# Optimization experiments

Measured on AMD Instinct MI355X. Metric: run time of the kernel, lower is better.

The kernel has to match this reference:

```python
import jax, jax.numpy as jnp
import numpy as np

B, N, D, H = 4, 2048, 256, 4
DH = D // H          # 64
SCALE = DH ** (-0.5)
LN_EPS = 1e-5


def setup_inputs() -> dict:
    key = jax.random.key(0)
    ks = jax.random.split(key, 16)
    g = lambda k, shape, fan_in: jax.random.normal(k, shape, jnp.float32) / np.sqrt(fan_in)
    # Weights stored as [in, out] (pre-transposed vs torch Linear)
    return {
        "x0": jax.random.normal(ks[0], (B, N, D), jnp.float32),
        "x1": jax.random.normal(ks[1], (B, N, D), jnp.float32),
        "Wqk": g(ks[2], (D, D), D), "bqk": jnp.zeros((D,), jnp.float32),
        "Wv": g(ks[3], (D, D), D), "bv": jnp.zeros((D,), jnp.float32),
        "Wout": g(ks[4], (D, D), D), "bout": jnp.zeros((D,), jnp.float32),
        "Wf1": g(ks[5], (2 * D, 2 * D), 2 * D), "bf1": jnp.zeros((2 * D,), jnp.float32),
        "ln_g": jnp.ones((2 * D,), jnp.float32), "ln_b": jnp.zeros((2 * D,), jnp.float32),
        "Wf2": g(ks[6], (2 * D, D), 2 * D), "bf2": jnp.zeros((D,), jnp.float32),
    }


def _split_heads(t):
    # [B,N,D] -> [B,H,N,DH]
    b, n, _ = t.shape
    return t.reshape(b, n, H, DH).transpose(0, 2, 1, 3)


def _merge_heads(t):
    # [B,H,N,DH] -> [B,N,D]
    b, h, n, dh = t.shape
    return t.transpose(0, 2, 1, 3).reshape(b, n, h * dh)


def _layernorm(x, g, b):
    mu = jnp.mean(x, axis=-1, keepdims=True)
    var = jnp.mean(jnp.square(x - mu), axis=-1, keepdims=True)
    return (x - mu) * jax.lax.rsqrt(var + LN_EPS) * g + b


def reference(x0, x1, Wqk, bqk, Wv, bv, Wout, bout, Wf1, bf1, ln_g, ln_b, Wf2, bf2):
    qk0 = _split_heads(x0 @ Wqk + bqk)   # [B,H,N,DH]
    qk1 = _split_heads(x1 @ Wqk + bqk)
    v0 = _split_heads(x0 @ Wv + bv)
    v1 = _split_heads(x1 @ Wv + bv)

    ss = SCALE ** 0.5
    sim = jnp.einsum('bhid,bhjd->bhij', qk0 * ss, qk1 * ss)  # shared score matrix
    attn01 = jax.nn.softmax(sim, axis=-1)   # normalize over j
    attn10 = jax.nn.softmax(sim, axis=-2)   # normalize over i (== softmax(sim^T) transposed)
    m0 = jnp.einsum('bhij,bhjd->bhid', attn01, v1)
    m1 = jnp.einsum('bhji,bhjd->bhid', attn10, v0)

    m0 = _merge_heads(m0) @ Wout + bout   # [B,N,D]
    m1 = _merge_heads(m1) @ Wout + bout

    def ffn(x):
        h = x @ Wf1 + bf1                 # [B,N,2D]
        h = jax.nn.gelu(_layernorm(h, ln_g, ln_b), approximate=False)
        return h @ Wf2 + bf2              # [B,N,D]

    y0 = x0 + ffn(jnp.concatenate([x0, m0], axis=-1))
    y1 = x1 + ffn(jnp.concatenate([x1, m1], axis=-1))
    return (y0, y1)
```

## Files before the change

kernel.cpp:

```cpp
#include <hip/hip_runtime.h>
#include <hip/hip_bf16.h>
#include <math.h>

typedef __bf16 bf16;
typedef __attribute__((ext_vector_type(8))) __bf16 bf16x8;
typedef __attribute__((ext_vector_type(4))) __bf16 bf16x4;
typedef __attribute__((ext_vector_type(2))) __bf16 bf16x2;
typedef __attribute__((ext_vector_type(4))) float f32x4;
typedef __attribute__((ext_vector_type(16))) float f32x16;
typedef __attribute__((ext_vector_type(4))) unsigned u32x4;

#define MFMA(a,b,c)   __builtin_amdgcn_mfma_f32_16x16x32_bf16(a,b,c,0,0,0)
#define MFMA32(a,b,c) __builtin_amdgcn_mfma_f32_32x32x16_bf16(a,b,c,0,0,0)

static constexpr int Bb = 4, Nn = 2048, Hh = 4;
static constexpr float SS2 = 0.4246609001440095f;

__device__ __forceinline__ void lds16(const bf16* src, bf16* dst) {
  __builtin_amdgcn_global_load_lds(
      (const __attribute__((address_space(1))) void*)src,
      (__attribute__((address_space(3))) void*)dst, 16, 0, 0);
}

__device__ __forceinline__ f32x16 zero16() {
  f32x16 t;
#pragma unroll
  for (int i = 0; i < 16; ++i) t[i] = 0.f;
  return t;
}

__global__ __launch_bounds__(256) void prep_k(
    const float* Wqk, const float* Wv, const float* Wout, const float* bout,
    const float* Wf1, const float* Wf2, const float* x0, const float* x1,
    bf16* wqkv_t, bf16* wout_b, bf16* wfold_t, bf16* wf1b_t, bf16* wf2_t,
    bf16* xb0, bf16* xb1) {
  int id = blockIdx.x * 256 + threadIdx.x;
  if (id < 65536) { int k = id >> 8, n = id & 255; wqkv_t[n*256 + k] = (bf16)Wqk[id]; return; }
  id -= 65536;
  if (id < 65536) { int k = id >> 8, n = id & 255; wqkv_t[(256 + n)*256 + k] = (bf16)Wv[id]; return; }
  id -= 65536;
  if (id < 98304) {
    if (id < 65536) { wout_b[id] = (bf16)Wout[id]; }
    else { int id3 = id - 65536; int r = id3 >> 8, k = id3 & 255;
           wout_b[(256 + r)*256 + k] = (r == 0) ? (bf16)bout[k] : (bf16)0.f; }
    return; }
  id -= 98304;
  if (id < 131072) { int o = id & 511, k = id >> 9; wfold_t[o*512 + k] = (bf16)Wf1[k*512 + o]; return; }
  id -= 131072;
  if (id < 131072) { int o = id & 511, k = id >> 9; wf1b_t[o*256 + k] = (bf16)Wf1[(256 + k)*512 + o]; return; }
  id -= 131072;
  if (id < 131072) { int k = id >> 8, n = id & 255; wf2_t[n*512 + k] = (bf16)Wf2[id]; return; }
  id -= 131072;
  if (id < 1048576) {
    const float* xs = (id < 524288) ? x0 : x1;
    bf16* xd = (id < 524288) ? xb0 : xb1;
    int j = (id < 524288) ? id : id - 524288;
    f32x4 v = *reinterpret_cast<const f32x4*>(&xs[(size_t)j * 4]);
    bf16x4 o; o[0] = (bf16)v[0]; o[1] = (bf16)v[1]; o[2] = (bf16)v[2]; o[3] = (bf16)v[3];
    *reinterpret_cast<bf16x4*>(&xd[(size_t)j * 4]) = o;
  }
}

template<int MODE, int BN, int MINW, int REMAP>
__global__ __launch_bounds__(256, MINW) void gemm_k(
    const bf16* Aa0, const bf16* Aa1, const bf16* Ac0, const bf16* Ac1,
    const bf16* Wt, const float* bias,
    bf16* ob0, bf16* ob1, float* of0, float* of1,
    const float* res0, const float* res1) {
  constexpr int KD  = (MODE == 3 || MODE == 4) ? 512 : 256;
  constexpr int LDA = (MODE == 4) ? 512 : 256;
  constexpr int NKC = KD / 64;
  constexpr int NF  = BN / 32;

  int bx = blockIdx.x, by = blockIdx.y, bz = blockIdx.z;
  if constexpr (REMAP) {
    int id = blockIdx.x + 64 * (blockIdx.y + 4 * blockIdx.z);
    bx = ((id & 7) << 3) + ((id >> 3) & 7);
    by = (id >> 6) & 3;
    bz = id >> 8;
  }

  const bf16* Aa = bz ? Aa1 : Aa0;
  const bf16* Ac = bz ? Ac1 : Ac0;
  bf16*  ob = bz ? ob1 : ob0;
  float* of = bz ? of1 : of0;
  const float* res = bz ? res1 : res0;

  const int tid = threadIdx.x;
  const int lane = tid & 63;
  const int w = tid >> 6;
  const int wr = w >> 1, wc = w & 1;
  const int m0r = bx * 128;
  const int n0 = by * BN;
  const int r15 = lane & 15, g = lane >> 4, rb = r15 & 7;
  const int l3 = lane >> 3, l7 = lane & 7;
  const int swzc = (l7 ^ l3) * 8;

  __shared__ bf16 At[2][8192];
  __shared__ bf16 Bt[2][BN * 64];

  const bf16* aA = Aa + (size_t)(m0r + w*32 + l3) * LDA + swzc;
  const bf16* aC = (MODE == 3) ? (Ac + (size_t)(m0r + w*32 + l3) * 256 + swzc) : nullptr;
  const bf16* bB = Wt + (size_t)(n0 + w*(BN/4) + l3) * KD + swzc;
  const int adst = (w*32) * 64;
  const int bdst = (w*(BN/4)) * 64;

  auto stage = [&](int buf, int kc) {
    const bf16* ab; int kcol;
    if constexpr (MODE == 3) {
      if (kc < 4) { ab = aA; kcol = kc * 64; } else { ab = aC; kcol = (kc - 4) * 64; }
    } else { ab = aA; kcol = kc * 64; }
#pragma unroll
    for (int i = 0; i < 4; i++)
      lds16(ab + kcol + (size_t)i * 8 * LDA, &At[buf][adst + i*512]);
#pragma unroll
    for (int i = 0; i < NF; i++)
      lds16(bB + kc*64 + (size_t)i * 8 * KD, &Bt[buf][bdst + i*512]);
  };

  f32x4 acc[4][NF];
#pragma unroll
  for (int i = 0; i < 4; i++)
#pragma unroll
    for (int j = 0; j < NF; j++) acc[i][j] = f32x4{0.f, 0.f, 0.f, 0.f};

  const int rx0 = ((0*4 + g) ^ rb) << 4;
  const int rx1 = ((1*4 + g) ^ rb) << 4;

  auto compute = [&](int cur) {
    const char* Ap = (const char*)&At[cur][0];
    const char* Bp = (const char*)&Bt[cur][0];
    __builtin_amdgcn_s_setprio(1);
#pragma unroll
    for (int ks = 0; ks < 2; ++ks) {
      const int rx = ks ? rx1 : rx0;
      bf16x8 af[4], bfr[NF];
#pragma unroll
      for (int mf = 0; mf < 4; ++mf)
        af[mf] = *reinterpret_cast<const bf16x8*>(Ap + (wr*64 + mf*16 + r15) * 128 + rx);
#pragma unroll
      for (int nf = 0; nf < NF; ++nf)
        bfr[nf] = *reinterpret_cast<const bf16x8*>(Bp + (wc*(BN/2) + nf*16 + r15) * 128 + rx);
#pragma unroll
      for (int mf = 0; mf < 4; ++mf)
#pragma unroll
        for (int nf = 0; nf < NF; ++nf)
          acc[mf][nf] = MFMA(af[mf], bfr[nf], acc[mf][nf]);
    }
    __builtin_amdgcn_s_setprio(0);
  };

  stage(0, 0);
  int cur = 0;
  for (int kc = 0; kc < NKC - 1; ++kc) {
    stage(cur ^ 1, kc + 1);
    if constexpr (NF == 4) asm volatile("s_waitcnt vmcnt(8)" ::: "memory");
    else                   asm volatile("s_waitcnt vmcnt(6)" ::: "memory");
    __builtin_amdgcn_sched_barrier(0);
    __builtin_amdgcn_s_barrier();
    __builtin_amdgcn_sched_barrier(0);
    compute(cur);
    asm volatile("s_waitcnt lgkmcnt(0)" ::: "memory");
    __builtin_amdgcn_sched_barrier(0);
    __builtin_amdgcn_s_barrier();
    __builtin_amdgcn_sched_barrier(0);
    cur ^= 1;
  }
  asm volatile("s_waitcnt vmcnt(0)" ::: "memory");
  __builtin_amdgcn_sched_barrier(0);
  __builtin_amdgcn_s_barrier();
  __builtin_amdgcn_sched_barrier(0);
  compute(cur);

#pragma unroll
  for (int mf = 0; mf < 4; ++mf)
#pragma unroll
    for (int nf = 0; nf < NF; ++nf) {
      f32x4 c = acc[mf][nf];
      int cg = n0 + wc*(BN/2) + nf*16 + r15;
#pragma unroll
      for (int r = 0; r < 4; ++r) {
        int rg = m0r + wr*64 + mf*16 + g*4 + r;
        if constexpr (MODE == 5) {
          int b = rg >> 11, n = rg & 2047;
          if (cg < 256) {
            float val = (c[r] + bias[cg]) * SS2;
            int h = cg >> 6, dh = cg & 63;
            ob[(((size_t)(b*Hh + h)) * Nn + n) * 64 + dh] = (bf16)val;
          } else {
            int c2 = cg - 256;
            float val = c[r] + res[c2];
            int h = c2 >> 6, dh = c2 & 63;
            ((bf16*)of)[(((size_t)(b*Hh + h)) * 64 + dh) * Nn + n] = (bf16)val;
          }
        } else if constexpr (MODE == 6) {
          if (rg < 256) ob[(size_t)cg * 512 + 256 + rg] = (bf16)c[r];
          else if (rg == 256) of[cg] = c[r] + bias[cg];
        } else if constexpr (MODE == 3) {
          ob[(size_t)rg * 512 + cg] = (bf16)(c[r] + bias[cg]);
        } else {
          of[(size_t)rg * 256 + cg] = c[r] + bias[cg] + (float)Ac[(size_t)rg * 256 + cg];
        }
      }
    }
}

__global__ __launch_bounds__(512, 4) void attn_k(
    const bf16* qks0, const bf16* qks1, const bf16* vT0, const bf16* vT1,
    bf16* m0o, bf16* m1o) {
  const int B = blockIdx.x + 16 * (blockIdx.y + 16 * blockIdx.z);
  const int xcd = B & 7, kk = B >> 3;
  const int group = 4 * xcd + (kk >> 4);
  const int it = kk & 15;
  const int bh = group & 15, dir = group >> 4;

  const bf16* Q  = (dir ? qks1 : qks0) + (size_t)bh * (Nn * 64);
  const bf16* Kp = (dir ? qks0 : qks1) + (size_t)bh * (Nn * 64);
  const bf16* Vp = (dir ? vT0  : vT1 ) + (size_t)bh * (64 * Nn);
  bf16* out = dir ? m1o : m0o;
  const int b = bh >> 2, h = bh & 3;

  const int tid = threadIdx.x, lane = tid & 63, w = tid >> 6;
  const int ig = w >> 1, hj = w & 1;
  const int l31 = lane & 31, hi = lane >> 5, xr = l31 & 7;
  const int iw = it * 128 + ig * 32;

  __shared__ char smem[65536];
  bf16* KV = (bf16*)smem;
  const int kbase = hj * 8192;
  const int vbase = 16384 + hj * 8192;

  bf16x8 qf[4];
#pragma unroll
  for (int kt = 0; kt < 4; ++kt)
    qf[kt] = *reinterpret_cast<const bf16x8*>(
        &Q[(size_t)(iw + l31) * 64 + kt*16 + hi*8]);

  bf16x8 ones;
#pragma unroll
  for (int i = 0; i < 8; ++i) ones[i] = (bf16)1.0f;

  f32x16 acc[2]; acc[0] = zero16(); acc[1] = zero16();
  f32x16 rsacc = zero16();

  const int l3 = lane >> 3, l7 = lane & 7;
  const int swz = ((l7 ^ l3) * 8);
  const bf16* ks0 = Kp + (size_t)(ig*16 +     l3) * 64 + swz;
  const bf16* ks1 = Kp + (size_t)(ig*16 + 8 + l3) * 64 + swz;
  const bf16* vs0 = Vp + (size_t)(ig*16 +     l3) * 2048 + swz;
  const bf16* vs1 = Vp + (size_t)(ig*16 + 8 + l3) * 2048 + swz;
  const int kd0 = (ig*16    ) * 64;
  const int kd1 = (ig*16 + 8) * 64;

  auto stage = [&](int buf, int j0) {
    lds16(ks0 + (size_t)j0 * 64, KV + kbase + buf*4096 + kd0);
    lds16(ks1 + (size_t)j0 * 64, KV + kbase + buf*4096 + kd1);
    lds16(vs0 + j0,              KV + vbase + buf*4096 + kd0);
    lds16(vs1 + j0,              KV + vbase + buf*4096 + kd1);
  };

  int kby[2][4], vby[2][4];
#pragma unroll
  for (int jm = 0; jm < 2; ++jm)
#pragma unroll
    for (int kt = 0; kt < 4; ++kt)
      kby[jm][kt] = (jm*32 + l31) * 128 + (((2*kt + hi) ^ xr) << 4);
#pragma unroll
  for (int nt = 0; nt < 2; ++nt)
#pragma unroll
    for (int gg = 0; gg < 4; ++gg)
      vby[nt][gg] = (nt*32 + l31) * 128 + (((2*gg + hi) ^ xr) << 4);

  auto compute_tile = [&](int cur) {
    const char* Kb = (const char*)(KV + kbase + cur*4096);
    const char* Vb = (const char*)(KV + vbase + cur*4096);
    f32x16 st[2];
    __builtin_amdgcn_s_setprio(1);
#pragma unroll
    for (int jm = 0; jm < 2; ++jm) {
      f32x16 t = zero16();
#pragma unroll
      for (int kt = 0; kt < 4; ++kt) {
        bf16x8 kf = *reinterpret_cast<const bf16x8*>(Kb + kby[jm][kt]);
        t = MFMA32(kf, qf[kt], t);
      }
      st[jm] = t;
    }
    __builtin_amdgcn_s_setprio(0);
    bf16x8 pa[4];
#pragma unroll
    for (int jm = 0; jm < 2; ++jm) {
      unsigned dw[8];
#pragma unroll
      for (int s = 0; s < 8; ++s) {
        float e0 = __builtin_amdgcn_exp2f(st[jm][2*s]);
        float e1 = __builtin_amdgcn_exp2f(st[jm][2*s + 1]);
        asm("v_cvt_pk_bf16_f32 %0, %1, %2" : "=v"(dw[s]) : "v"(e0), "v"(e1));
      }
#pragma unroll
      for (int kt2 = 0; kt2 < 2; ++kt2) {
        unsigned a0 = dw[4*kt2 + 0], b0 = dw[4*kt2 + 2];
        unsigned a1 = dw[4*kt2 + 1], b1 = dw[4*kt2 + 3];
        asm volatile("v_permlane32_swap_b32 %0, %1" : "+v"(a0), "+v"(b0));
        asm volatile("v_permlane32_swap_b32 %0, %1" : "+v"(a1), "+v"(b1));
        u32x4 uu; uu[0] = a0; uu[1] = a1; uu[2] = b0; uu[3] = b1;
        pa[jm*2 + kt2] = __builtin_bit_cast(bf16x8, uu);
      }
    }
    __builtin_amdgcn_s_setprio(1);
#pragma unroll
    for (int gg = 0; gg < 4; ++gg) {
      rsacc = MFMA32(pa[gg], ones, rsacc);
#pragma unroll
      for (int nt = 0; nt < 2; ++nt) {
        bf16x8 vf = *reinterpret_cast<const bf16x8*>(Vb + vby[nt][gg]);
        acc[nt] = MFMA32(pa[gg], vf, acc[nt]);
      }
    }
    __builtin_amdgcn_s_setprio(0);
  };

  const int jt0 = hj << 4;
  stage(0, jt0 << 6);
  int cur = 0;
  for (int t = 0; t < 15; ++t) {
    stage(cur ^ 1, (jt0 + t + 1) << 6);
    asm volatile("s_waitcnt vmcnt(4)" ::: "memory");
    __builtin_amdgcn_sched_barrier(0);
    __builtin_amdgcn_s_barrier();
    __builtin_amdgcn_sched_barrier(0);
    compute_tile(cur);
    asm volatile("s_waitcnt lgkmcnt(0)" ::: "memory");
    __builtin_amdgcn_sched_barrier(0);
    __builtin_amdgcn_s_barrier();
    __builtin_amdgcn_sched_barrier(0);
    cur ^= 1;
  }
  asm volatile("s_waitcnt vmcnt(0)" ::: "memory");
  __builtin_amdgcn_sched_barrier(0);
  __builtin_amdgcn_s_barrier();
  __builtin_amdgcn_sched_barrier(0);
  compute_tile(cur);

  __syncthreads();
  float* Ex = (float*)smem;
  if (hj == 1) {
#pragma unroll
    for (int nt = 0; nt < 2; ++nt)
#pragma unroll
      for (int r = 0; r < 16; ++r)
        Ex[(ig*48 + nt*16 + r) * 64 + lane] = acc[nt][r];
#pragma unroll
    for (int r = 0; r < 16; ++r)
      Ex[(ig*48 + 32 + r) * 64 + lane] = rsacc[r];
  }
  __syncthreads();
  if (hj == 0) {
#pragma unroll
    for (int r = 0; r < 16; ++r) {
      float rs = rsacc[r] + Ex[(ig*48 + 32 + r) * 64 + lane];
      float inv = 1.0f / rs;
      int row = iw + (r & 3) + 8*(r >> 2) + 4*hi;
#pragma unroll
      for (int nt = 0; nt < 2; ++nt) {
        float o = acc[nt][r] + Ex[(ig*48 + nt*16 + r) * 64 + lane];
        int col = h*64 + nt*32 + l31;
        out[((size_t)b * Nn + row) * 256 + col] = (bf16)(o * inv);
      }
    }
  }
}

__global__ __launch_bounds__(256) void ln_gelu_k(
    bf16* hg, const float* g, const float* bb) {
  const int row = (blockIdx.x << 2) + (threadIdx.x >> 6);
  const int lane = threadIdx.x & 63;
  bf16* hr = hg + (size_t)row * 512 + lane * 8;
  bf16x8 v = *reinterpret_cast<const bf16x8*>(hr);
  float f[8];
  float s = 0.f, sq = 0.f;
#pragma unroll
  for (int i = 0; i < 8; ++i) { f[i] = (float)v[i]; s += f[i]; sq += f[i]*f[i]; }
#pragma unroll
  for (int m = 1; m < 64; m <<= 1) { s += __shfl_xor(s, m); sq += __shfl_xor(sq, m); }
  float mu = s * (1.f / 512.f);
  float var = sq * (1.f / 512.f) - mu * mu;
  float rsv = rsqrtf(var + 1e-5f);
  f32x4 g0 = *reinterpret_cast<const f32x4*>(&g[lane*8]);
  f32x4 g1 = *reinterpret_cast<const f32x4*>(&g[lane*8 + 4]);
  f32x4 b0 = *reinterpret_cast<const f32x4*>(&bb[lane*8]);
  f32x4 b1 = *reinterpret_cast<const f32x4*>(&bb[lane*8 + 4]);
  bf16x8 o;
#pragma unroll
  for (int i = 0; i < 8; ++i) {
    float gv = (i < 4) ? g0[i] : g1[i-4];
    float bv = (i < 4) ? b0[i] : b1[i-4];
    float xn = (f[i] - mu) * rsv * gv + bv;
    float ge = 0.5f * xn * (1.f + erff(xn * 0.70710678118f));
    o[i] = (bf16)ge;
  }
  *reinterpret_cast<bf16x8*>(hr) = o;
}

extern "C" void kernel_launch(void* const* d_in, const int* in_sizes, int n_in,
                              void* d_out, int out_size, void* d_ws, size_t ws_size,
                              hipStream_t stream) {
  (void)in_sizes; (void)n_in; (void)out_size; (void)ws_size;
  const float* x0   = (const float*)d_in[0];
  const float* x1   = (const float*)d_in[1];
  const float* Wqk  = (const float*)d_in[2];
  const float* bqk  = (const float*)d_in[3];
  const float* Wv   = (const float*)d_in[4];
  const float* bv   = (const float*)d_in[5];
  const float* Wout = (const float*)d_in[6];
  const float* bout = (const float*)d_in[7];
  const float* Wf1  = (const float*)d_in[8];
  const float* bf1  = (const float*)d_in[9];
  const float* ln_g = (const float*)d_in[10];
  const float* ln_b = (const float*)d_in[11];
  const float* Wf2  = (const float*)d_in[12];
  const float* bf2  = (const float*)d_in[13];
  float* y = (float*)d_out;

  bf16* p = (bf16*)d_ws;
  bf16* wqkv_t = p; p += 131072;
  bf16* wout_b = p; p += 98304;
  bf16* wfold_t = p; p += 262144;
  bf16* wf1b_t = p; p += 131072;
  bf16* wf2_t  = p; p += 131072;
  float* bfold = (float*)p; p += 1024;
  bf16* xb0  = p; p += 2097152;
  bf16* xb1  = p; p += 2097152;
  bf16* qks0 = p; p += 2097152;
  bf16* qks1 = p; p += 2097152;
  bf16* vT0  = p; p += 2097152;
  bf16* vT1  = p; p += 2097152;
  bf16* m0   = p; p += 2097152;
  bf16* m1   = p; p += 2097152;
  bf16* hg0  = p; p += 4194304;
  bf16* hg1  = p; p += 4194304;

  dim3 blk(256);
  prep_k<<<6528, blk, 0, stream>>>(Wqk, Wv, Wout, bout, Wf1, Wf2, x0, x1,
                                   wqkv_t, wout_b, wfold_t, wf1b_t, wf2_t, xb0, xb1);
  gemm_k<6,128,2,0><<<dim3(3, 4, 1), blk, 0, stream>>>(
      wout_b, wout_b, nullptr, nullptr, wf1b_t, bf1,
      wfold_t, wfold_t, bfold, bfold, nullptr, nullptr);
  gemm_k<5,128,2,1><<<dim3(64, 4, 2), blk, 0, stream>>>(
      xb0, xb1, nullptr, nullptr, wqkv_t, bqk,
      qks0, qks1, (float*)vT0, (float*)vT1, bv, bv);
  attn_k<<<dim3(16, 16, 2), dim3(512), 0, stream>>>(qks0, qks1, vT0, vT1, m0, m1);
  gemm_k<3,128,2,1><<<dim3(64, 4, 2), blk, 0, stream>>>(
      xb0, xb1, m0, m1, wfold_t, bfold,
      hg0, hg1, nullptr, nullptr, nullptr, nullptr);
  ln_gelu_k<<<dim3(4096), blk, 0, stream>>>(hg0, ln_g, ln_b);
  gemm_k<4,64,3,1><<<dim3(64, 4, 2), blk, 0, stream>>>(
      hg0, hg1, xb0, xb1, wf2_t, bf2,
      nullptr, nullptr, y, y + 2097152, nullptr, nullptr);
}
```

Measured before the change: 129.4 us.

## Tile weight transposes through LDS and widen final FFN GEMM tiles

The prep kernel now transposes weight matrices in 64x64 tiles staged through shared memory, so both global reads and writes are coalesced and vectorized. The Wout conversion and the x casts get packed per-thread work, which cuts the grid from 6528 to 4320 blocks. The final Wf2 GEMM moves from BN=64 with 3 waves/SIMD to BN=128 with 2, using a new block remap for the 64x2x2 grid. That halves the number of blocks and re-reads of A, at the cost of occupancy and fewer blocks to spread across CUs.

After: 131.7 us. Within noise of the previous version (+1.8%).

```diff
diff --git a/kernel.cpp b/kernel.cpp
--- a/kernel.cpp
+++ b/kernel.cpp
@@ -34,30 +34,68 @@
     const float* Wf1, const float* Wf2, const float* x0, const float* x1,
     bf16* wqkv_t, bf16* wout_b, bf16* wfold_t, bf16* wf1b_t, bf16* wf2_t,
     bf16* xb0, bf16* xb1) {
-  int id = blockIdx.x * 256 + threadIdx.x;
-  if (id < 65536) { int k = id >> 8, n = id & 255; wqkv_t[n*256 + k] = (bf16)Wqk[id]; return; }
-  id -= 65536;
-  if (id < 65536) { int k = id >> 8, n = id & 255; wqkv_t[(256 + n)*256 + k] = (bf16)Wv[id]; return; }
-  id -= 65536;
-  if (id < 98304) {
-    if (id < 65536) { wout_b[id] = (bf16)Wout[id]; }
-    else { int id3 = id - 65536; int r = id3 >> 8, k = id3 & 255;
-           wout_b[(256 + r)*256 + k] = (r == 0) ? (bf16)bout[k] : (bf16)0.f; }
-    return; }
-  id -= 98304;
-  if (id < 131072) { int o = id & 511, k = id >> 9; wfold_t[o*512 + k] = (bf16)Wf1[k*512 + o]; return; }
-  id -= 131072;
-  if (id < 131072) { int o = id & 511, k = id >> 9; wf1b_t[o*256 + k] = (bf16)Wf1[(256 + k)*512 + o]; return; }
-  id -= 131072;
-  if (id < 131072) { int k = id >> 8, n = id & 255; wf2_t[n*512 + k] = (bf16)Wf2[id]; return; }
-  id -= 131072;
-  if (id < 1048576) {
-    const float* xs = (id < 524288) ? x0 : x1;
-    bf16* xd = (id < 524288) ? xb0 : xb1;
-    int j = (id < 524288) ? id : id - 524288;
-    f32x4 v = *reinterpret_cast<const f32x4*>(&xs[(size_t)j * 4]);
+  const int bid = blockIdx.x, tid = threadIdx.x;
+  if (bid < 128) {
+    __shared__ float LT[64][65];
+    const float* src; bf16* dst;
+    int srcLD, dstLD, r0, c0, rbase;
+    int t = bid;
+    if (t < 16) {
+      src = Wqk; srcLD = 256; r0 = (t >> 2) * 64; c0 = (t & 3) * 64;
+      dst = wqkv_t; dstLD = 256; rbase = 0;
+    } else if (t < 32) { t -= 16;
+      src = Wv; srcLD = 256; r0 = (t >> 2) * 64; c0 = (t & 3) * 64;
+      dst = wqkv_t + 256 * 256; dstLD = 256; rbase = 0;
+    } else if (t < 64) { t -= 32;
+      src = Wf1; srcLD = 512; r0 = (t >> 3) * 64; c0 = (t & 7) * 64;
+      dst = wfold_t; dstLD = 512; rbase = 0;
+    } else if (t < 96) { t -= 64;
+      src = Wf1; srcLD = 512; r0 = 256 + (t >> 3) * 64; c0 = (t & 7) * 64;
+      dst = wf1b_t; dstLD = 256; rbase = 256;
+    } else { t -= 96;
+      src = Wf2; srcLD = 256; r0 = (t >> 2) * 64; c0 = (t & 3) * 64;
+      dst = wf2_t; dstLD = 512; rbase = 0;
+    }
+#pragma unroll
+    for (int i = 0; i < 4; ++i) {
+      int rr = (tid >> 4) + i * 16;
+      int cc = (tid & 15) * 4;
+      f32x4 v = *reinterpret_cast<const f32x4*>(&src[(size_t)(r0 + rr) * srcLD + c0 + cc]);
+      LT[rr][cc] = v[0]; LT[rr][cc + 1] = v[1]; LT[rr][cc + 2] = v[2]; LT[rr][cc + 3] = v[3];
+    }
+    __syncthreads();
+    int n = tid >> 2, kc = (tid & 3) * 16;
+    bf16x8 o0, o1;
+#pragma unroll
+    for (int i = 0; i < 8; ++i) o0[i] = (bf16)LT[kc + i][n];
+#pragma unroll
+    for (int i = 0; i < 8; ++i) o1[i] = (bf16)LT[kc + 8 + i][n];
+    bf16* dp = dst + (size_t)(c0 + n) * dstLD + (r0 - rbase) + kc;
+    *reinterpret_cast<bf16x8*>(dp) = o0;
+    *reinterpret_cast<bf16x8*>(dp + 8) = o1;
+    return;
+  }
+  int id = bid - 128;
+  if (id < 96) {
+    int base = id * 1024 + tid * 4;
+#pragma unroll
+    for (int i = 0; i < 4; ++i) {
+      int e = base + i;
+      if (e < 65536) wout_b[e] = (bf16)Wout[e];
+      else { int id3 = e - 65536; int r = id3 >> 8, k = id3 & 255;
+             wout_b[e] = (r == 0) ? (bf16)bout[k] : (bf16)0.f; }
+    }
+    return;
+  }
+  id -= 96;
+  if (id < 4096) {
+    int j = id * 256 + tid;
+    const float* xs = (j < 524288) ? x0 : x1;
+    bf16* xd = (j < 524288) ? xb0 : xb1;
+    int jj = (j < 524288) ? j : j - 524288;
+    f32x4 v = *reinterpret_cast<const f32x4*>(&xs[(size_t)jj * 4]);
     bf16x4 o; o[0] = (bf16)v[0]; o[1] = (bf16)v[1]; o[2] = (bf16)v[2]; o[3] = (bf16)v[3];
-    *reinterpret_cast<bf16x4*>(&xd[(size_t)j * 4]) = o;
+    *reinterpret_cast<bf16x4*>(&xd[(size_t)jj * 4]) = o;
   }
 }
 
@@ -73,11 +111,16 @@
   constexpr int NF  = BN / 32;
 
   int bx = blockIdx.x, by = blockIdx.y, bz = blockIdx.z;
-  if constexpr (REMAP) {
+  if constexpr (REMAP == 1) {
     int id = blockIdx.x + 64 * (blockIdx.y + 4 * blockIdx.z);
     bx = ((id & 7) << 3) + ((id >> 3) & 7);
     by = (id >> 6) & 3;
     bz = id >> 8;
+  } else if constexpr (REMAP == 2) {
+    int id = blockIdx.x + 64 * (blockIdx.y + 2 * blockIdx.z);
+    bx = ((id & 7) << 3) + ((id >> 3) & 7);
+    by = (id >> 6) & 1;
+    bz = id >> 7;
   }
 
   const bf16* Aa = bz ? Aa1 : Aa0;
@@ -441,7 +484,7 @@
   bf16* hg1  = p; p += 4194304;
 
   dim3 blk(256);
-  prep_k<<<6528, blk, 0, stream>>>(Wqk, Wv, Wout, bout, Wf1, Wf2, x0, x1,
+  prep_k<<<4320, blk, 0, stream>>>(Wqk, Wv, Wout, bout, Wf1, Wf2, x0, x1,
                                    wqkv_t, wout_b, wfold_t, wf1b_t, wf2_t, xb0, xb1);
   gemm_k<6,128,2,0><<<dim3(3, 4, 1), blk, 0, stream>>>(
       wout_b, wout_b, nullptr, nullptr, wf1b_t, bf1,
@@ -454,7 +497,7 @@
       xb0, xb1, m0, m1, wfold_t, bfold,
       hg0, hg1, nullptr, nullptr, nullptr, nullptr);
   ln_gelu_k<<<dim3(4096), blk, 0, stream>>>(hg0, ln_g, ln_b);
-  gemm_k<4,64,3,1><<<dim3(64, 4, 2), blk, 0, stream>>>(
+  gemm_k<4,128,2,2><<<dim3(64, 2, 2), blk, 0, stream>>>(
       hg0, hg1, xb0, xb1, wf2_t, bf2,
       nullptr, nullptr, y, y + 2097152, nullptr, nullptr);
 }
```
